# Performance work log

Measured on AMD Instinct MI355X. Metric: run time of the kernel, lower is better.

The kernel has to match this reference:

```python
import jax, jax.numpy as jnp
import numpy as np

# Config (lite version of KimiK2): 2 layers, dim 2048, 16 heads x 128, MLA latent rank 512,
# 4 experts / top-2, SwiGLU inter dim 1024, vocab 32000, batch 2, seq 1024.
DEPTH, DIM, H, HD, R, DFF, E, TOPK, V, B, S = 2, 2048, 16, 128, 512, 1024, 4, 2, 32000, 2, 1024
EPS = 1e-6


def rmsnorm(x, w):
    var = jnp.mean(jnp.square(x), axis=-1, keepdims=True)
    return x * jax.lax.rsqrt(var + EPS) * w


def setup_inputs() -> dict:
    key = jax.random.key(0)
    ks = jax.random.split(key, 16)
    sd = 0.02
    d = {
        'x_tokens': jax.random.randint(ks[0], (B, S), 0, V),
        'emb': jax.random.normal(ks[1], (V, DIM), jnp.float32) * sd,
        'embed_norm_w': jnp.ones((DIM,), jnp.float32),
        # per-layer stacked params (leading axis DEPTH)
        'norm_w': jnp.ones((DEPTH, DIM), jnp.float32),
        'Wq': jax.random.normal(ks[2], (DEPTH, DIM, H * HD), jnp.float32) * sd,
        'Wdkv': jax.random.normal(ks[3], (DEPTH, DIM, R), jnp.float32) * sd,
        'Wuk': jax.random.normal(ks[4], (DEPTH, R, H * HD), jnp.float32) * sd,
        'Wuv': jax.random.normal(ks[5], (DEPTH, R, H * HD), jnp.float32) * sd,
        'Wo': jax.random.normal(ks[6], (DEPTH, H * HD, DIM), jnp.float32) * sd,
        'Wg': jax.random.normal(ks[7], (DEPTH, DIM, E), jnp.float32) * sd,
        'W1': jax.random.normal(ks[8], (DEPTH, E, DIM, DFF), jnp.float32) * sd,
        'W3': jax.random.normal(ks[9], (DEPTH, E, DIM, DFF), jnp.float32) * sd,
        'W2': jax.random.normal(ks[10], (DEPTH, E, DFF, DIM), jnp.float32) * sd,
        'head_norm_w': jnp.ones((DIM,), jnp.float32),
        'head_W': jax.random.normal(ks[11], (DIM, V), jnp.float32) * sd,
        'head_b': jnp.zeros((V,), jnp.float32),
    }
    return d


def mla(x, Wq, Wdkv, Wuk, Wuv, Wo):
    # Multi-head latent attention: queries from x, K/V from a low-rank latent c.
    Bq, Sq, _ = x.shape
    q = (x @ Wq).reshape(Bq, Sq, H, HD)
    c = x @ Wdkv                                   # [B,S,R] compressed KV latent
    k = (c @ Wuk).reshape(Bq, Sq, H, HD)
    v = (c @ Wuv).reshape(Bq, Sq, H, HD)
    scores = jnp.einsum('bqhd,bkhd->bhqk', q, k) / jnp.sqrt(jnp.float32(HD))
    a = jax.nn.softmax(scores, axis=-1)            # block never passes a mask -> full attention
    o = jnp.einsum('bhqk,bkhd->bqhd', a, v).reshape(Bq, Sq, H * HD)
    return o @ Wo


def moe(x, Wg, W1, W3, W2):
    # x: [B,S,D] -> flatten tokens. Dense-over-experts (E=4) with top-k masked gates.
    Bq, Sq, Dq = x.shape
    xt = x.reshape(Bq * Sq, Dq)                    # [T,D]
    gate = jax.nn.softmax(xt @ Wg, axis=-1)        # [T,E]
    topv, topi = jax.lax.top_k(gate, TOPK)
    topv = topv / jnp.sum(topv, axis=-1, keepdims=True)
    gw = jnp.zeros_like(gate).at[jnp.arange(xt.shape[0])[:, None], topi].set(topv)  # [T,E]
    h = jnp.einsum('td,edf->etf', xt, W1)
    g = jnp.einsum('td,edf->etf', xt, W3)
    eo = jnp.einsum('etf,efd->etd', jax.nn.silu(h) * g, W2)
    out = jnp.einsum('etd,te->td', eo, gw)
    return out.reshape(Bq, Sq, Dq)


def reference(x_tokens, emb, embed_norm_w, norm_w, Wq, Wdkv, Wuk, Wuv, Wo, Wg, W1, W3, W2, head_norm_w, head_W, head_b):
    h = emb[x_tokens]
    h = rmsnorm(h, embed_norm_w)

    def layer(h, p):
        nw, wq, wdkv, wuk, wuv, wo, wg, w1, w3, w2 = p
        h = h + mla(rmsnorm(h, nw), wq, wdkv, wuk, wuv, wo)
        # NOTE: same norm weight reused pre-MoE, as in the torch module
        h = h + moe(rmsnorm(h, nw), wg, w1, w3, w2)
        return h, None

    h, _ = jax.lax.scan(layer, h, (norm_w, Wq, Wdkv, Wuk, Wuv, Wo, Wg, W1, W3, W2))
    return rmsnorm(h, head_norm_w) @ head_W + head_b
```

## Files before the change

kernel.cpp:

```cpp
#include <hip/hip_runtime.h>
#include <hip/hip_bf16.h>

typedef __hip_bfloat16 bf16;
typedef __bf16 bf16x8 __attribute__((ext_vector_type(8)));
typedef float f32x4 __attribute__((ext_vector_type(4)));
typedef unsigned short u16;
typedef unsigned int u32;
typedef __attribute__((address_space(1))) const void* gptr_t;
typedef __attribute__((address_space(3))) void* lptr_t;

static constexpr int TOKS = 2048, DM = 2048, RL = 512, DF = 1024, SQ = 1024, NV = 32000;
static constexpr int CAP = 1536;
static constexpr long PL_X  = (long)TOKS * DM;
static constexpr long PL_C  = (long)TOKS * RL;
static constexpr long PL_VT = 2l * 16 * 128 * 1024;
static constexpr long M4 = 4l * 1024 * 1024;
static constexpr long M2 = 2l * 1024 * 1024;

__device__ __forceinline__ float b2f(bf16 x){ return __bfloat162float(x); }
__device__ __forceinline__ bf16  f2b(float x){ return __float2bfloat16(x); }
__device__ __forceinline__ void split1(float x, u16& h, u16& l){
  bf16 hb = f2b(x);
  float r = x - b2f(hb);
  bf16 lb = f2b(r);
  h = *(u16*)&hb; l = *(u16*)&lb;
}

__device__ __forceinline__ float block_red(float v, int op){
  __shared__ float red[4];
  const int lane = threadIdx.x & 63, wv = threadIdx.x >> 6;
  #pragma unroll
  for (int off = 32; off > 0; off >>= 1){
    float o = __shfl_down(v, off, 64);
    v = op ? fmaxf(v, o) : v + o;
  }
  __syncthreads();
  if (lane == 0) red[wv] = v;
  __syncthreads();
  float r = red[0];
  #pragma unroll
  for (int i = 1; i < 4; ++i) r = op ? fmaxf(r, red[i]) : r + red[i];
  return r;
}

__global__ __launch_bounds__(256)
void embed_norm_k(const int* __restrict__ toks, const float* __restrict__ emb,
                  const float* __restrict__ w, float* __restrict__ h){
  const int t = blockIdx.x;
  const long tok = toks[t];
  const int base = threadIdx.x * 8;
  const float* ep = emb + tok * (long)DM + base;
  float4 va = *(const float4*)ep, vb = *(const float4*)(ep + 4);
  float v[8] = {va.x, va.y, va.z, va.w, vb.x, vb.y, vb.z, vb.w};
  float ss = 0.f;
  #pragma unroll
  for (int i = 0; i < 8; ++i) ss += v[i]*v[i];
  ss = block_red(ss, 0);
  const float inv = rsqrtf(ss / DM + 1e-6f);
  float4 wa = *(const float4*)(w + base), wb4 = *(const float4*)(w + base + 4);
  float wv[8] = {wa.x, wa.y, wa.z, wa.w, wb4.x, wb4.y, wb4.z, wb4.w};
  float* hp = h + (long)t * DM + base;
  #pragma unroll
  for (int i = 0; i < 8; ++i) hp[i] = v[i] * inv * wv[i];
}

__global__ __launch_bounds__(256)
void rmsnorm_planes_k(const float* __restrict__ h, const float* __restrict__ w,
                      u16* __restrict__ hi, u16* __restrict__ lo){
  const int t = blockIdx.x;
  const int base = threadIdx.x * 8;
  const float* hp = h + (long)t * DM + base;
  float4 va = *(const float4*)hp, vb = *(const float4*)(hp + 4);
  float v[8] = {va.x, va.y, va.z, va.w, vb.x, vb.y, vb.z, vb.w};
  float ss = 0.f;
  #pragma unroll
  for (int i = 0; i < 8; ++i) ss += v[i]*v[i];
  ss = block_red(ss, 0);
  const float inv = rsqrtf(ss / DM + 1e-6f);
  float4 wa = *(const float4*)(w + base), wb4 = *(const float4*)(w + base + 4);
  float wv[8] = {wa.x, wa.y, wa.z, wa.w, wb4.x, wb4.y, wb4.z, wb4.w};
  u16 hvv[8], lvv[8];
  #pragma unroll
  for (int i = 0; i < 8; ++i) split1(v[i] * inv * wv[i], hvv[i], lvv[i]);
  *(int4*)(hi + (long)t * DM + base) = *(const int4*)hvv;
  *(int4*)(lo + (long)t * DM + base) = *(const int4*)lvv;
}

__global__ __launch_bounds__(256)
void gate_k(const float* __restrict__ h, const float* __restrict__ nw,
            const float* __restrict__ Wg, float* __restrict__ gw){
  const int t = blockIdx.x;
  const int base = threadIdx.x * 8;
  const float* hp = h + (long)t * DM + base;
  float4 va = *(const float4*)hp, vb = *(const float4*)(hp + 4);
  float v[8] = {va.x, va.y, va.z, va.w, vb.x, vb.y, vb.z, vb.w};
  float ss = 0.f;
  #pragma unroll
  for (int i = 0; i < 8; ++i) ss += v[i]*v[i];
  ss = block_red(ss, 0);
  const float inv = rsqrtf(ss / DM + 1e-6f);
  float a[4] = {0.f, 0.f, 0.f, 0.f};
  #pragma unroll
  for (int i = 0; i < 8; ++i){
    const float xv = v[i] * inv * nw[base + i];
    #pragma unroll
    for (int e = 0; e < 4; ++e) a[e] += xv * Wg[(base + i)*4 + e];
  }
  #pragma unroll
  for (int e = 0; e < 4; ++e) a[e] = block_red(a[e], 0);
  if (threadIdx.x == 0){
    int i1 = 0;
    for (int e = 1; e < 4; ++e) if (a[e] > a[i1]) i1 = e;
    int i2 = -1;
    for (int e = 0; e < 4; ++e){ if (e == i1) continue; if (i2 < 0 || a[e] > a[i2]) i2 = e; }
    float g[4];
    const float m = fmaxf(fmaxf(a[0], a[1]), fmaxf(a[2], a[3]));
    float s = 0.f;
    for (int e = 0; e < 4; ++e){ g[e] = __expf(a[e] - m); s += g[e]; }
    for (int e = 0; e < 4; ++e) g[e] /= s;
    const float ns = g[i1] + g[i2];
    float* op = gw + (long)t * 4;
    op[0] = 0.f; op[1] = 0.f; op[2] = 0.f; op[3] = 0.f;
    op[i1] = g[i1] / ns; op[i2] = g[i2] / ns;
  }
}

__global__ __launch_bounds__(256)
void build_lists_k(const float* __restrict__ gw, int* __restrict__ idx, int* __restrict__ cnt){
  const int e = threadIdx.x >> 6, lane = threadIdx.x & 63;
  int base = 0;
  for (int t0 = 0; t0 < TOKS; t0 += 64){
    const int t = t0 + lane;
    const bool sel = gw[(long)t * 4 + e] > 0.f;
    const unsigned long long m = __ballot(sel);
    const int pos = __popcll(m & ((1ull << lane) - 1ull));
    if (sel && base + pos < CAP) idx[e * CAP + base + pos] = t;
    base += (int)__popcll(m);
  }
  if (lane == 0) cnt[e] = base < CAP ? base : CAP;
}

__global__ __launch_bounds__(256)
void gather2_k(const u16* __restrict__ xph, const int* __restrict__ idx,
               const int* __restrict__ cnt, int ebase, u16* __restrict__ xg){
  const int e = blockIdx.x / CAP, r = blockIdx.x % CAP;
  if (r >= cnt[ebase + e]) return;
  const long t = idx[(long)(ebase + e) * CAP + r];
  const int c = threadIdx.x * 8;
  const long dst = ((long)e * 2 * CAP + r) * DM + c;
  *(int4*)(xg + dst) = *(const int4*)(xph + t * DM + c);
  *(int4*)(xg + dst + (long)CAP * DM) = *(const int4*)(xph + PL_X + t * DM + c);
}

__global__ __launch_bounds__(256)
void gatherb_k(const u16* __restrict__ xph, const int* __restrict__ idx,
               const int* __restrict__ cnt, u16* __restrict__ xgb){
  const int e = blockIdx.x / CAP, r = blockIdx.x % CAP;
  if (r >= cnt[e]) return;
  const long t = idx[(long)e * CAP + r];
  const int c = threadIdx.x * 8;
  *(int4*)(xgb + ((long)e * CAP + r) * DM + c) = *(const int4*)(xph + t * DM + c);
}

__global__ __launch_bounds__(256)
void softmax_pack_k(float* __restrict__ pf){
  const long row = blockIdx.x;
  const float* pr = pf + row * SQ;
  const int base = threadIdx.x * 4;
  float4 v4 = *(const float4*)(pr + base);
  float v[4] = {v4.x, v4.y, v4.z, v4.w};
  float m = fmaxf(fmaxf(v[0], v[1]), fmaxf(v[2], v[3]));
  m = block_red(m, 1);
  float s = 0.f;
  #pragma unroll
  for (int i = 0; i < 4; ++i){ v[i] = __expf(v[i] - m); s += v[i]; }
  s = block_red(s, 0);
  const float inv = 1.f / s;
  u16 hv[4], lv[4];
  #pragma unroll
  for (int i = 0; i < 4; ++i) split1(v[i] * inv, hv[i], lv[i]);
  u16* out = (u16*)pf + row * 2048;
  *(int2*)(out + base) = *(const int2*)hv;
  *(int2*)(out + 1024 + base) = *(const int2*)lv;
}

__global__ __launch_bounds__(256)
void swiglu_pack_k(float* __restrict__ h1, const float* __restrict__ h3){
  const int t = threadIdx.x;
  const long r = (long)blockIdx.x * 2 + (t >> 7);
  const int col = (t & 127) * 8;
  const float* p1 = h1 + r * 1024 + col;
  const float* p3 = h3 + r * 1024 + col;
  float4 a0 = *(const float4*)p1, a1 = *(const float4*)(p1 + 4);
  float4 b0 = *(const float4*)p3, b1 = *(const float4*)(p3 + 4);
  float a[8] = {a0.x, a0.y, a0.z, a0.w, a1.x, a1.y, a1.z, a1.w};
  float b[8] = {b0.x, b0.y, b0.z, b0.w, b1.x, b1.y, b1.z, b1.w};
  u16 hv[8], lv[8];
  #pragma unroll
  for (int j = 0; j < 8; ++j){
    const float y = (a[j] / (1.f + __expf(-a[j]))) * b[j];
    split1(y, hv[j], lv[j]);
  }
  __syncthreads();
  u16* out = (u16*)h1 + r * 2048;
  *(int4*)(out + col) = *(const int4*)hv;
  *(int4*)(out + 1024 + col) = *(const int4*)lv;
}

__global__ __launch_bounds__(256)
void swiglu_bk(bf16* __restrict__ h1, const bf16* __restrict__ h3){
  const long i = ((long)blockIdx.x * 256 + threadIdx.x) * 8;
  union { int4 i4; bf16 b[8]; } x, y;
  x.i4 = *(const int4*)(h1 + i);
  y.i4 = *(const int4*)(h3 + i);
  #pragma unroll
  for (int j = 0; j < 8; ++j){
    const float a = b2f(x.b[j]);
    const float b = b2f(y.b[j]);
    x.b[j] = f2b((a / (1.f + __expf(-a))) * b);
  }
  *(int4*)(h1 + i) = x.i4;
}

__global__ __launch_bounds__(256)
void tsplit_k(const float* __restrict__ in, long inz, int ldin,
              u16* __restrict__ oh, u16* __restrict__ ol, long outz, int ldout, int ntx){
  __shared__ u16 lh[64][72], ll[64][72];
  const int z = blockIdx.z;
  in += (long)z * inz; oh += (long)z * outz; ol += (long)z * outz;
  const int bx = blockIdx.x % ntx, by = blockIdx.x / ntx;
  const int k0 = by * 64, n0 = bx * 64;
  const int t = threadIdx.x;
  {
    const int r = t >> 2, cb = (t & 3) * 16;
    const float* ip = in + (long)(k0 + r) * ldin + n0 + cb;
    #pragma unroll
    for (int i = 0; i < 16; i += 4){
      float4 v = *(const float4*)(ip + i);
      float a[4] = {v.x, v.y, v.z, v.w};
      #pragma unroll
      for (int j = 0; j < 4; ++j){
        u16 hv, lv; split1(a[j], hv, lv);
        lh[r][cb + i + j] = hv; ll[r][cb + i + j] = lv;
      }
    }
  }
  __syncthreads();
  {
    const int n = t >> 2, kb = (t & 3) * 16;
    u16 hv[16], lv[16];
    #pragma unroll
    for (int i = 0; i < 16; ++i){ hv[i] = lh[kb + i][n]; lv[i] = ll[kb + i][n]; }
    u16* po = oh + (long)(n0 + n) * ldout + k0 + kb;
    u16* pl = ol + (long)(n0 + n) * ldout + k0 + kb;
    *(int4*)po = *(const int4*)hv; *(int4*)(po + 8) = *(const int4*)(hv + 8);
    *(int4*)pl = *(const int4*)lv; *(int4*)(pl + 8) = *(const int4*)(lv + 8);
  }
}

__global__ __launch_bounds__(256)
void tconv_k(const float* __restrict__ in, long inz, int ldin,
             bf16* __restrict__ out, long outz, int ldout, int ntx){
  __shared__ u16 lh[64][72];
  const int z = blockIdx.z;
  in += (long)z * inz; out += (long)z * outz;
  const int bx = blockIdx.x % ntx, by = blockIdx.x / ntx;
  const int k0 = by * 64, n0 = bx * 64;
  const int t = threadIdx.x;
  {
    const int r = t >> 2, cb = (t & 3) * 16;
    const float* ip = in + (long)(k0 + r) * ldin + n0 + cb;
    #pragma unroll
    for (int i = 0; i < 16; i += 4){
      float4 v = *(const float4*)(ip + i);
      float a[4] = {v.x, v.y, v.z, v.w};
      #pragma unroll
      for (int j = 0; j < 4; ++j){ bf16 hb = f2b(a[j]); lh[r][cb + i + j] = *(u16*)&hb; }
    }
  }
  __syncthreads();
  {
    const int n = t >> 2, kb = (t & 3) * 16;
    u16 hv[16];
    #pragma unroll
    for (int i = 0; i < 16; ++i) hv[i] = lh[kb + i][n];
    u16* po = (u16*)out + (long)(n0 + n) * ldout + k0 + kb;
    *(int4*)po = *(const int4*)hv; *(int4*)(po + 8) = *(const int4*)(hv + 8);
  }
}

__device__ __forceinline__ int swz2(int r, int c){
  return ((((c >> 3) + (r >> 1)) & 3) << 3) | (c & 7);
}
__device__ __forceinline__ int2 tile_xy(int ny){
  const int nwg = gridDim.x;
  const int wid = blockIdx.x;
  const int q = nwg >> 3, r = nwg & 7;
  const int xcd = wid & 7, pos = wid >> 3;
  const int lid = (xcd < r) ? (xcd*(q+1) + pos) : (r*(q+1) + (xcd - r)*q + pos);
  return make_int2(lid / ny, lid % ny);
}

__device__ __forceinline__ void stage_issue(const u16* src, int ld, int rbase, int k0,
                                            u16* lp, int sub, int lane){
  const int r = sub * 16 + (lane >> 2);
  const int cs = ((lane & 3) - (r >> 1)) & 3;
  const u16* g = src + (long)(rbase + r) * ld + k0 + cs * 8;
  __builtin_amdgcn_global_load_lds((gptr_t)g, (lptr_t)(lp + sub * 512), 16, 0, 0);
}

template<int MT, int OM>
__global__ __launch_bounds__(256)
void gemms_nt(const u16* __restrict__ Ah, const u16* __restrict__ Al, long ab, int lda,
              const u16* __restrict__ Bh, const u16* __restrict__ Bl, long bb, int ldb,
              void* __restrict__ Cv, long cb, int ldc, long cpl,
              int K, float scale, const float* __restrict__ aux, int gst, int ny,
              const int* __restrict__ rowmap, const int* __restrict__ cntp)
{
  __shared__ __align__(16) u16 ash[MT*32][32], asl[MT*32][32];
  __shared__ __align__(16) u16 bsh[128][32], bsl[128][32];
  const int z = blockIdx.z;
  Ah += (long)z * ab; Al += (long)z * ab;
  Bh += (long)z * bb; Bl += (long)z * bb;
  const int2 tt = tile_xy(ny);
  const int m0 = tt.y * (MT*32), n0 = tt.x * 128;
  int cntv = 1 << 30;
  if (cntp){ cntv = cntp[z]; if (m0 >= cntv) return; }
  const int tid = threadIdx.x, lane = tid & 63, wv = tid >> 6;
  const int wr = (wv >> 1) * (MT*16), wc = (wv & 1) * 64;
  const int fr = lane & 15, fk = (lane >> 4) * 8;

  f32x4 acc[MT][4] = {};
  constexpr int AI = MT * 2;

  for (int k0 = 0; k0 < K; k0 += 32){
    __syncthreads();
    #pragma unroll
    for (int ii = 0; ii < 2*AI + 16; ++ii){
      if ((ii & 3) != wv) continue;
      if (ii < AI)            stage_issue(Ah, lda, m0, k0, &ash[0][0], ii, lane);
      else if (ii < 2*AI)     stage_issue(Al, lda, m0, k0, &asl[0][0], ii - AI, lane);
      else if (ii < 2*AI + 8) stage_issue(Bh, ldb, n0, k0, &bsh[0][0], ii - 2*AI, lane);
      else                    stage_issue(Bl, ldb, n0, k0, &bsl[0][0], ii - 2*AI - 8, lane);
    }
    __syncthreads();
    bf16x8 ahf[MT], alf[MT], bhf[4], blf[4];
    #pragma unroll
    for (int mi = 0; mi < MT; ++mi){
      const int rr = wr + mi * 16 + fr;
      const int sc = swz2(rr, fk);
      ahf[mi] = *(const bf16x8*)&ash[rr][sc];
      alf[mi] = *(const bf16x8*)&asl[rr][sc];
    }
    #pragma unroll
    for (int ni = 0; ni < 4; ++ni){
      const int rr = wc + ni * 16 + fr;
      const int sc = swz2(rr, fk);
      bhf[ni] = *(const bf16x8*)&bsh[rr][sc];
      blf[ni] = *(const bf16x8*)&bsl[rr][sc];
    }
    #pragma unroll
    for (int mi = 0; mi < MT; ++mi)
      #pragma unroll
      for (int ni = 0; ni < 4; ++ni){
        acc[mi][ni] = __builtin_amdgcn_mfma_f32_16x16x32_bf16(ahf[mi], bhf[ni], acc[mi][ni], 0, 0, 0);
        acc[mi][ni] = __builtin_amdgcn_mfma_f32_16x16x32_bf16(ahf[mi], blf[ni], acc[mi][ni], 0, 0, 0);
        acc[mi][ni] = __builtin_amdgcn_mfma_f32_16x16x32_bf16(alf[mi], bhf[ni], acc[mi][ni], 0, 0, 0);
      }
  }

  const int crow = (lane >> 4) * 4, ccol = lane & 15;
  #pragma unroll
  for (int mi = 0; mi < MT; ++mi){
    #pragma unroll
    for (int ni = 0; ni < 4; ++ni){
      const int gm0 = m0 + wr + mi * 16 + crow;
      const int gn = n0 + wc + ni * 16 + ccol;
      if (OM == 5){
        u16 hv[4], lv[4];
        #pragma unroll
        for (int j = 0; j < 4; ++j) split1(acc[mi][ni][j], hv[j], lv[j]);
        const long off = (((long)(gm0 >> 10) * 16 + (gn >> 7)) * 128 + (gn & 127)) * 1024 + (gm0 & 1023);
        u16* vt = (u16*)Cv;
        *(int2*)(vt + off) = *(const int2*)hv;
        *(int2*)(vt + cpl + off) = *(const int2*)lv;
      } else if (OM == 6){
        #pragma unroll
        for (int j = 0; j < 4; ++j){
          const int row = gm0 + j;
          if (row < cntv){
            const long t = rowmap[(long)z * CAP + row];
            ((float*)Cv)[t * ldc + gn] += aux[t * gst] * acc[mi][ni][j];
          }
        }
      } else {
        #pragma unroll
        for (int j = 0; j < 4; ++j){
          const long off = (long)z * cb + (long)(gm0 + j) * ldc + gn;
          const float v = acc[mi][ni][j];
          if (OM == 0)      ((float*)Cv)[off] = v * scale;
          else if (OM == 1) ((float*)Cv)[off] += v;
          else if (OM == 3) ((float*)Cv)[off] += aux[(long)(gm0 + j) * gst] * v;
          else { u16 hv, lv; split1(v, hv, lv); ((u16*)Cv)[off] = hv; ((u16*)Cv)[off + cpl] = lv; }
        }
      }
    }
  }
}

template<int MT, int OM>
__global__ __launch_bounds__(256)
void gemmb_nt(const bf16* __restrict__ A, long ab, int lda,
              const bf16* __restrict__ B, long bb, int ldb,
              void* __restrict__ Cv, long cb, int ldc,
              int K, const float* __restrict__ aux, int gst, int ny,
              const int* __restrict__ rowmap, const int* __restrict__ cntp)
{
  __shared__ __align__(16) u16 a_lds[MT*32][32];
  __shared__ __align__(16) u16 b_lds[128][32];
  const int z = blockIdx.z;
  A += (long)z * ab; B += (long)z * bb;
  const int2 tt = tile_xy(ny);
  const int m0 = tt.y * (MT*32), n0 = tt.x * 128;
  int cntv = 1 << 30;
  if (cntp){ cntv = cntp[z]; if (m0 >= cntv) return; }
  const int tid = threadIdx.x, lane = tid & 63, wv = tid >> 6;
  const int wr = (wv >> 1) * (MT*16), wc = (wv & 1) * 64;
  const int fr = lane & 15, fk = (lane >> 4) * 8;

  f32x4 acc[MT][4] = {};
  constexpr int AI = MT * 2;

  for (int k0 = 0; k0 < K; k0 += 32){
    __syncthreads();
    #pragma unroll
    for (int ii = 0; ii < AI + 8; ++ii){
      if ((ii & 3) != wv) continue;
      if (ii < AI) stage_issue((const u16*)A, lda, m0, k0, &a_lds[0][0], ii, lane);
      else         stage_issue((const u16*)B, ldb, n0, k0, &b_lds[0][0], ii - AI, lane);
    }
    __syncthreads();
    bf16x8 af[MT], bfv[4];
    #pragma unroll
    for (int mi = 0; mi < MT; ++mi){
      const int rr = wr + mi * 16 + fr;
      af[mi] = *(const bf16x8*)&a_lds[rr][swz2(rr, fk)];
    }
    #pragma unroll
    for (int ni = 0; ni < 4; ++ni){
      const int rr = wc + ni * 16 + fr;
      bfv[ni] = *(const bf16x8*)&b_lds[rr][swz2(rr, fk)];
    }
    #pragma unroll
    for (int mi = 0; mi < MT; ++mi)
      #pragma unroll
      for (int ni = 0; ni < 4; ++ni)
        acc[mi][ni] = __builtin_amdgcn_mfma_f32_16x16x32_bf16(af[mi], bfv[ni], acc[mi][ni], 0, 0, 0);
  }

  const int crow = (lane >> 4) * 4, ccol = lane & 15;
  #pragma unroll
  for (int mi = 0; mi < MT; ++mi){
    #pragma unroll
    for (int ni = 0; ni < 4; ++ni){
      const int gm0 = m0 + wr + mi * 16 + crow;
      const int gn = n0 + wc + ni * 16 + ccol;
      #pragma unroll
      for (int j = 0; j < 4; ++j){
        const float v = acc[mi][ni][j];
        if (OM == 7){
          const int row = gm0 + j;
          if (row < cntv){
            const long t = rowmap[(long)z * CAP + row];
            atomicAdd(&((float*)Cv)[t * ldc + gn], aux[t * gst + z] * v);
          }
        } else {
          const long off = (long)z * cb + (long)(gm0 + j) * ldc + gn;
          if (OM == 0)      ((bf16*)Cv)[off] = f2b(v);
          else if (OM == 2) ((float*)Cv)[off] = v + aux[gn];
          else              atomicAdd(&((float*)Cv)[off], aux[(long)(gm0 + j) * gst + z] * v);
        }
      }
    }
  }
}

extern "C" void kernel_launch(void* const* d_in, const int* in_sizes, int n_in,
                              void* d_out, int out_size, void* d_ws, size_t ws_size,
                              hipStream_t stream)
{
  (void)in_sizes; (void)n_in; (void)out_size; (void)ws_size;
  const int*   toks = (const int*)d_in[0];
  const float* emb  = (const float*)d_in[1];
  const float* enw  = (const float*)d_in[2];
  const float* nw   = (const float*)d_in[3];
  const float* Wq   = (const float*)d_in[4];
  const float* Wdkv = (const float*)d_in[5];
  const float* Wuk  = (const float*)d_in[6];
  const float* Wuv  = (const float*)d_in[7];
  const float* Wo   = (const float*)d_in[8];
  const float* Wg   = (const float*)d_in[9];
  const float* W1   = (const float*)d_in[10];
  const float* W3   = (const float*)d_in[11];
  const float* W2   = (const float*)d_in[12];
  const float* hnw  = (const float*)d_in[13];
  const float* hW   = (const float*)d_in[14];
  const float* hb   = (const float*)d_in[15];

  const size_t MB = 1ull << 20;
  char* ws = (char*)d_ws;
  float* h    = (float*)(ws);
  float* gw   = (float*)(ws + 16*MB);
  int*   idx  = (int*)(ws + 16*MB + 128*1024);
  int*   cnt  = (int*)(ws + 16*MB + 256*1024);
  u16*   xph  = (u16*)(ws + 17*MB);
  u16*   wpl  = (u16*)(ws + 33*MB);
  u16*   qph  = (u16*)(ws + 49*MB);
  u16*   cph  = (u16*)(ws + 65*MB);
  u16*   kph  = (u16*)(ws + 69*MB);
  u16*   vtp  = (u16*)(ws + 85*MB);
  u16*   oph  = (u16*)(ws + 101*MB);
  float* pf   = (float*)(ws + 17*MB);
  u16*   xg   = (u16*)(ws + 49*MB);
  float* h1f  = (float*)(ws + 73*MB);
  float* h3f  = (float*)(ws + 85*MB);
  bf16*  wT   = (bf16*)(ws + 33*MB);
  u16*   xgb  = (u16*)(ws + 49*MB);
  bf16*  h1b  = (bf16*)(ws + 73*MB);
  bf16*  h3b  = (bf16*)(ws + 85*MB);
  bf16*  whT  = (bf16*)(ws + 33*MB);

  const float qscale = 0.08838834764831845f;

  embed_norm_k<<<TOKS, 256, 0, stream>>>(toks, emb, enw, h);

  for (int l = 0; l < 2; ++l){
    const float* nwl = nw + (long)l * DM;
    rmsnorm_planes_k<<<TOKS, 256, 0, stream>>>(h, nwl, xph, xph + PL_X);

    tsplit_k<<<1024, 256, 0, stream>>>(Wq + (long)l*DM*DM, 0, DM, wpl, wpl + M4, 0, DM, 32);
    gemms_nt<2,4><<<dim3(512,1,1), 256, 0, stream>>>(xph, xph + PL_X, 0, DM, wpl, wpl + M4, 0, DM,
        qph, 0, DM, PL_X, DM, 1.f, nullptr, 0, 32, nullptr, nullptr);
    tsplit_k<<<256, 256, 0, stream>>>(Wdkv + (long)l*DM*RL, 0, RL, wpl, wpl + M2, 0, DM, 8);
    gemms_nt<2,4><<<dim3(128,1,1), 256, 0, stream>>>(xph, xph + PL_X, 0, DM, wpl, wpl + M2, 0, DM,
        cph, 0, RL, PL_C, DM, 1.f, nullptr, 0, 32, nullptr, nullptr);
    tsplit_k<<<256, 256, 0, stream>>>(Wuk + (long)l*RL*DM, 0, DM, wpl, wpl + M2, 0, RL, 32);
    gemms_nt<2,4><<<dim3(512,1,1), 256, 0, stream>>>(cph, cph + PL_C, 0, RL, wpl, wpl + M2, 0, RL,
        kph, 0, DM, PL_X, RL, 1.f, nullptr, 0, 32, nullptr, nullptr);
    tsplit_k<<<256, 256, 0, stream>>>(Wuv + (long)l*RL*DM, 0, DM, wpl, wpl + M2, 0, RL, 32);
    gemms_nt<2,5><<<dim3(512,1,1), 256, 0, stream>>>(cph, cph + PL_C, 0, RL, wpl, wpl + M2, 0, RL,
        vtp, 0, 0, PL_VT, RL, 1.f, nullptr, 0, 32, nullptr, nullptr);

    for (int b = 0; b < 2; ++b){
      for (int hg = 0; hg < 2; ++hg){
        const long qo = (long)b*SQ*DM + hg*1024;
        gemms_nt<4,0><<<dim3(64,1,8), 256, 0, stream>>>(qph + qo, qph + PL_X + qo, 128, DM,
            kph + qo, kph + PL_X + qo, 128, DM,
            pf, (long)SQ*SQ, SQ, 0, 128, qscale, nullptr, 0, 8, nullptr, nullptr);
        softmax_pack_k<<<8*SQ, 256, 0, stream>>>(pf);
        const long vo = ((long)b*16 + hg*8) * 128 * 1024;
        gemms_nt<1,4><<<dim3(32,1,8), 256, 0, stream>>>((const u16*)pf, (const u16*)pf + 1024,
            1024l*2048, 2048,
            vtp + vo, vtp + PL_VT + vo, 128l*1024, 1024,
            oph + (long)b*SQ*DM + hg*1024, 128, DM, PL_X, SQ, 1.f, nullptr, 0, 32, nullptr, nullptr);
      }
    }

    tsplit_k<<<1024, 256, 0, stream>>>(Wo + (long)l*DM*DM, 0, DM, wpl, wpl + M4, 0, DM, 32);
    gemms_nt<2,1><<<dim3(512,1,1), 256, 0, stream>>>(oph, oph + PL_X, 0, DM, wpl, wpl + M4, 0, DM,
        h, 0, DM, 0, DM, 1.f, nullptr, 0, 32, nullptr, nullptr);

    gate_k<<<TOKS, 256, 0, stream>>>(h, nwl, Wg + (long)l*DM*4, gw);
    build_lists_k<<<1, 256, 0, stream>>>(gw, idx, cnt);
    rmsnorm_planes_k<<<TOKS, 256, 0, stream>>>(h, nwl, xph, xph + PL_X);

    if (l == 0){
      for (int p2 = 0; p2 < 2; ++p2){
        const int ebase = p2 * 2;
        const long wo13 = ((long)l*4 + ebase) * (long)DM * DF;
        gather2_k<<<2*CAP, 256, 0, stream>>>(xph, idx, cnt, ebase, xg);
        tsplit_k<<<dim3(512,1,2), 256, 0, stream>>>(W1 + wo13, (long)DM*DF, DF, wpl, wpl + M4, M2, DM, 16);
        gemms_nt<2,0><<<dim3(192,1,2), 256, 0, stream>>>(xg, xg + (long)CAP*DM, 2l*CAP*DM, DM,
            wpl, wpl + M4, M2, DM, h1f, (long)CAP*DF, DF, 0, DM, 1.f, nullptr, 0, 24,
            nullptr, cnt + ebase);
        tsplit_k<<<dim3(512,1,2), 256, 0, stream>>>(W3 + wo13, (long)DM*DF, DF, wpl, wpl + M4, M2, DM, 16);
        gemms_nt<2,0><<<dim3(192,1,2), 256, 0, stream>>>(xg, xg + (long)CAP*DM, 2l*CAP*DM, DM,
            wpl, wpl + M4, M2, DM, h3f, (long)CAP*DF, DF, 0, DM, 1.f, nullptr, 0, 24,
            nullptr, cnt + ebase);
        swiglu_pack_k<<<CAP, 256, 0, stream>>>(h1f, h3f);
        tsplit_k<<<dim3(512,1,2), 256, 0, stream>>>(W2 + ((long)l*4 + ebase)*(long)DF*DM, (long)DF*DM, DM,
            wpl, wpl + M4, M2, DF, 32);
        for (int ei = 0; ei < 2; ++ei){
          gemms_nt<2,6><<<dim3(384,1,1), 256, 0, stream>>>(
              (const u16*)h1f + (long)ei*CAP*2048, (const u16*)h1f + (long)ei*CAP*2048 + 1024,
              0, 2048, wpl + (long)ei*M2, wpl + M4 + (long)ei*M2, 0, DF,
              h, 0, DM, 0, DF, 1.f, gw + ebase + ei, 4, 24,
              idx + (ebase + ei)*CAP, cnt + ebase + ei);
        }
      }
    } else {
      gatherb_k<<<4*CAP, 256, 0, stream>>>(xph, idx, cnt, xgb);
      tconv_k<<<dim3(512,1,4), 256, 0, stream>>>(W1 + (long)l*4*DM*DF, (long)DM*DF, DF, wT, M2, DM, 16);
      gemmb_nt<2,0><<<dim3(192,1,4), 256, 0, stream>>>((const bf16*)xgb, (long)CAP*DM, DM, wT, M2, DM,
          h1b, (long)CAP*DF, DF, DM, nullptr, 0, 24, nullptr, cnt);
      tconv_k<<<dim3(512,1,4), 256, 0, stream>>>(W3 + (long)l*4*DM*DF, (long)DM*DF, DF, wT, M2, DM, 16);
      gemmb_nt<2,0><<<dim3(192,1,4), 256, 0, stream>>>((const bf16*)xgb, (long)CAP*DM, DM, wT, M2, DM,
          h3b, (long)CAP*DF, DF, DM, nullptr, 0, 24, nullptr, cnt);
      swiglu_bk<<<(4*CAP*DF)/2048, 256, 0, stream>>>(h1b, h3b);
      tconv_k<<<dim3(512,1,4), 256, 0, stream>>>(W2 + (long)l*4*DF*DM, (long)DF*DM, DM, wT, M2, DF, 32);
      gemmb_nt<2,7><<<dim3(384,1,4), 256, 0, stream>>>(h1b, (long)CAP*DF, DF, wT, M2, DF,
          h, 0, DM, DF, gw, 4, 24, idx, cnt);
    }
  }

  rmsnorm_planes_k<<<TOKS, 256, 0, stream>>>(h, hnw, xph, xph + PL_X);
  for (int half = 0; half < 2; ++half){
    tconv_k<<<8000, 256, 0, stream>>>(hW + half*16000, 0, NV, whT, 0, DM, 250);
    gemmb_nt<4,2><<<dim3(2000,1,1), 256, 0, stream>>>((const bf16*)xph, 0, DM, whT, 0, DM,
        (float*)d_out + half*16000, 0, NV, DM, hb + half*16000, 0, 16, nullptr, nullptr);
  }
}
```

Baseline: 2.291 ms.

## Double-buffer LDS staging in split and bf16 GEMM kernels to overlap loads

Both GEMM kernels now keep two LDS buffers and issue the async global-to-LDS loads for the next K tile before computing on the current one. Partial s_waitcnt vmcnt plus raw barriers replace the two __syncthreads per iteration, so memory latency can overlap the MFMA work. The attention score GEMM also moves from MT=4 to MT=2 tiles with twice the grid, which gives more workgroups and less LDS per block. The cost is double the LDS footprint, which may lower occupancy, and hand-written waitcnt logic that depends on each wave issuing exactly IPW loads.

```diff
diff --git a/kernel.cpp b/kernel.cpp
--- a/kernel.cpp
+++ b/kernel.cpp
@@ -309,6 +309,23 @@
   __builtin_amdgcn_global_load_lds((gptr_t)g, (lptr_t)(lp + sub * 512), 16, 0, 0);
 }
 
+template<int N> __device__ __forceinline__ void wait_vmcnt(){
+  if constexpr (N == 0) asm volatile("s_waitcnt vmcnt(0)" ::: "memory");
+  else if constexpr (N == 3) asm volatile("s_waitcnt vmcnt(3)" ::: "memory");
+  else if constexpr (N == 4) asm volatile("s_waitcnt vmcnt(4)" ::: "memory");
+  else if constexpr (N == 5) asm volatile("s_waitcnt vmcnt(5)" ::: "memory");
+  else if constexpr (N == 6) asm volatile("s_waitcnt vmcnt(6)" ::: "memory");
+  else if constexpr (N == 8) asm volatile("s_waitcnt vmcnt(8)" ::: "memory");
+  __builtin_amdgcn_sched_barrier(0);
+}
+__device__ __forceinline__ void barrier_raw(){
+  __builtin_amdgcn_sched_barrier(0);
+  asm volatile("" ::: "memory");
+  __builtin_amdgcn_s_barrier();
+  asm volatile("" ::: "memory");
+  __builtin_amdgcn_sched_barrier(0);
+}
+
 template<int MT, int OM>
 __global__ __launch_bounds__(256)
 void gemms_nt(const u16* __restrict__ Ah, const u16* __restrict__ Al, long ab, int lda,
@@ -317,8 +334,8 @@
               int K, float scale, const float* __restrict__ aux, int gst, int ny,
               const int* __restrict__ rowmap, const int* __restrict__ cntp)
 {
-  __shared__ __align__(16) u16 ash[MT*32][32], asl[MT*32][32];
-  __shared__ __align__(16) u16 bsh[128][32], bsl[128][32];
+  __shared__ __align__(16) u16 ash[2][MT*32][32], asl[2][MT*32][32];
+  __shared__ __align__(16) u16 bsh[2][128][32], bsl[2][128][32];
   const int z = blockIdx.z;
   Ah += (long)z * ab; Al += (long)z * ab;
   Bh += (long)z * bb; Bl += (long)z * bb;
@@ -332,32 +349,40 @@
 
   f32x4 acc[MT][4] = {};
   constexpr int AI = MT * 2;
-
+  constexpr int TOT = 2*AI + 16;
+  constexpr int IPW = TOT / 4;
+
+  auto STAGE = [&](int bf, int k0){
+    #pragma unroll
+    for (int ii = 0; ii < TOT; ++ii){
+      if ((ii & 3) != wv) continue;
+      if (ii < AI)            stage_issue(Ah, lda, m0, k0, &ash[bf][0][0], ii, lane);
+      else if (ii < 2*AI)     stage_issue(Al, lda, m0, k0, &asl[bf][0][0], ii - AI, lane);
+      else if (ii < 2*AI + 8) stage_issue(Bh, ldb, n0, k0, &bsh[bf][0][0], ii - 2*AI, lane);
+      else                    stage_issue(Bl, ldb, n0, k0, &bsl[bf][0][0], ii - 2*AI - 8, lane);
+    }
+  };
+
+  STAGE(0, 0);
+  int cur = 0;
   for (int k0 = 0; k0 < K; k0 += 32){
-    __syncthreads();
-    #pragma unroll
-    for (int ii = 0; ii < 2*AI + 16; ++ii){
-      if ((ii & 3) != wv) continue;
-      if (ii < AI)            stage_issue(Ah, lda, m0, k0, &ash[0][0], ii, lane);
-      else if (ii < 2*AI)     stage_issue(Al, lda, m0, k0, &asl[0][0], ii - AI, lane);
-      else if (ii < 2*AI + 8) stage_issue(Bh, ldb, n0, k0, &bsh[0][0], ii - 2*AI, lane);
-      else                    stage_issue(Bl, ldb, n0, k0, &bsl[0][0], ii - 2*AI - 8, lane);
-    }
-    __syncthreads();
+    if (k0 + 32 < K){ STAGE(cur ^ 1, k0 + 32); wait_vmcnt<IPW>(); }
+    else              wait_vmcnt<0>();
+    barrier_raw();
     bf16x8 ahf[MT], alf[MT], bhf[4], blf[4];
     #pragma unroll
     for (int mi = 0; mi < MT; ++mi){
       const int rr = wr + mi * 16 + fr;
       const int sc = swz2(rr, fk);
-      ahf[mi] = *(const bf16x8*)&ash[rr][sc];
-      alf[mi] = *(const bf16x8*)&asl[rr][sc];
+      ahf[mi] = *(const bf16x8*)&ash[cur][rr][sc];
+      alf[mi] = *(const bf16x8*)&asl[cur][rr][sc];
     }
     #pragma unroll
     for (int ni = 0; ni < 4; ++ni){
       const int rr = wc + ni * 16 + fr;
       const int sc = swz2(rr, fk);
-      bhf[ni] = *(const bf16x8*)&bsh[rr][sc];
-      blf[ni] = *(const bf16x8*)&bsl[rr][sc];
+      bhf[ni] = *(const bf16x8*)&bsh[cur][rr][sc];
+      blf[ni] = *(const bf16x8*)&bsl[cur][rr][sc];
     }
     #pragma unroll
     for (int mi = 0; mi < MT; ++mi)
@@ -367,6 +392,8 @@
         acc[mi][ni] = __builtin_amdgcn_mfma_f32_16x16x32_bf16(ahf[mi], blf[ni], acc[mi][ni], 0, 0, 0);
         acc[mi][ni] = __builtin_amdgcn_mfma_f32_16x16x32_bf16(alf[mi], bhf[ni], acc[mi][ni], 0, 0, 0);
       }
+    barrier_raw();
+    cur ^= 1;
   }
 
   const int crow = (lane >> 4) * 4, ccol = lane & 15;
@@ -416,8 +443,8 @@
               int K, const float* __restrict__ aux, int gst, int ny,
               const int* __restrict__ rowmap, const int* __restrict__ cntp)
 {
-  __shared__ __align__(16) u16 a_lds[MT*32][32];
-  __shared__ __align__(16) u16 b_lds[128][32];
+  __shared__ __align__(16) u16 a_lds[2][MT*32][32];
+  __shared__ __align__(16) u16 b_lds[2][128][32];
   const int z = blockIdx.z;
   A += (long)z * ab; B += (long)z * bb;
   const int2 tt = tile_xy(ny);
@@ -430,32 +457,42 @@
 
   f32x4 acc[MT][4] = {};
   constexpr int AI = MT * 2;
-
+  constexpr int TOT = AI + 8;
+  constexpr int IPW = TOT / 4;
+
+  auto STAGE = [&](int bf, int k0){
+    #pragma unroll
+    for (int ii = 0; ii < TOT; ++ii){
+      if ((ii & 3) != wv) continue;
+      if (ii < AI) stage_issue((const u16*)A, lda, m0, k0, &a_lds[bf][0][0], ii, lane);
+      else         stage_issue((const u16*)B, ldb, n0, k0, &b_lds[bf][0][0], ii - AI, lane);
+    }
+  };
+
+  STAGE(0, 0);
+  int cur = 0;
   for (int k0 = 0; k0 < K; k0 += 32){
-    __syncthreads();
-    #pragma unroll
-    for (int ii = 0; ii < AI + 8; ++ii){
-      if ((ii & 3) != wv) continue;
-      if (ii < AI) stage_issue((const u16*)A, lda, m0, k0, &a_lds[0][0], ii, lane);
-      else         stage_issue((const u16*)B, ldb, n0, k0, &b_lds[0][0], ii - AI, lane);
-    }
-    __syncthreads();
+    if (k0 + 32 < K){ STAGE(cur ^ 1, k0 + 32); wait_vmcnt<IPW>(); }
+    else              wait_vmcnt<0>();
+    barrier_raw();
     bf16x8 af[MT], bfv[4];
     #pragma unroll
     for (int mi = 0; mi < MT; ++mi){
       const int rr = wr + mi * 16 + fr;
-      af[mi] = *(const bf16x8*)&a_lds[rr][swz2(rr, fk)];
+      af[mi] = *(const bf16x8*)&a_lds[cur][rr][swz2(rr, fk)];
     }
     #pragma unroll
     for (int ni = 0; ni < 4; ++ni){
       const int rr = wc + ni * 16 + fr;
-      bfv[ni] = *(const bf16x8*)&b_lds[rr][swz2(rr, fk)];
+      bfv[ni] = *(const bf16x8*)&b_lds[cur][rr][swz2(rr, fk)];
     }
     #pragma unroll
     for (int mi = 0; mi < MT; ++mi)
       #pragma unroll
       for (int ni = 0; ni < 4; ++ni)
         acc[mi][ni] = __builtin_amdgcn_mfma_f32_16x16x32_bf16(af[mi], bfv[ni], acc[mi][ni], 0, 0, 0);
+    barrier_raw();
+    cur ^= 1;
   }
 
   const int crow = (lane >> 4) * 4, ccol = lane & 15;
@@ -554,9 +591,9 @@
     for (int b = 0; b < 2; ++b){
       for (int hg = 0; hg < 2; ++hg){
         const long qo = (long)b*SQ*DM + hg*1024;
-        gemms_nt<4,0><<<dim3(64,1,8), 256, 0, stream>>>(qph + qo, qph + PL_X + qo, 128, DM,
+        gemms_nt<2,0><<<dim3(128,1,8), 256, 0, stream>>>(qph + qo, qph + PL_X + qo, 128, DM,
             kph + qo, kph + PL_X + qo, 128, DM,
-            pf, (long)SQ*SQ, SQ, 0, 128, qscale, nullptr, 0, 8, nullptr, nullptr);
+            pf, (long)SQ*SQ, SQ, 0, 128, qscale, nullptr, 0, 16, nullptr, nullptr);
         softmax_pack_k<<<8*SQ, 256, 0, stream>>>(pf);
         const long vo = ((long)b*16 + hg*8) * 128 * 1024;
         gemms_nt<1,4><<<dim3(32,1,8), 256, 0, stream>>>((const u16*)pf, (const u16*)pf + 1024,
```

Measured after the change: 2.328 ms. No clear change (+1.6%).
